# Kernel tuning notes

Measured on AMD Instinct MI355X. Metric: run time of the kernel, lower is better.

## Reference

```python
import jax, jax.numpy as jnp
import numpy as np


def setup_inputs() -> dict:
    key = jax.random.key(0)
    k1, k2, k3 = jax.random.split(key, 3)
    B, C, H, W = 4, 32, 256, 256
    nw, nh = 16, 16
    K = nw * nh
    pixel_feats = jax.random.normal(k1, (B, C, H, W), dtype=jnp.float32)
    assoc_map = jax.random.uniform(k2, (B, 9, H, W), dtype=jnp.float32)
    index_map = jax.random.randint(k3, (B, H, W), 0, K, dtype=jnp.int32)
    return {
        "pixel_feats": pixel_feats,
        "assoc_map": assoc_map,
        "index_map": index_map,
        "nw_spixels": nw,
        "nh_spixels": nh,
    }


def reference(pixel_feats, assoc_map, index_map, nw_spixels, nh_spixels):
    # pixel_feats: [B,C,H,W], assoc_map: [B,9,H,W] (3x3 superpixel-neighbor
    # association weights, row-major (dy,dx) in {-1,0,1}^2), index_map: [B,H,W]
    # base superpixel id in [0, nw*nh). Output: [B, C, nw*nh].
    B, C, H, W = pixel_feats.shape
    K = nw_spixels * nh_spixels
    P = H * W

    idx = index_map.reshape(B, P).astype(jnp.int32)
    ix = idx % nw_spixels  # base spixel grid x
    iy = idx // nw_spixels  # base spixel grid y

    # 9 relative offsets over the superpixel grid
    dy, dx = jnp.meshgrid(jnp.arange(-1, 2), jnp.arange(-1, 2), indexing="ij")
    dy = dy.reshape(9)
    dx = dx.reshape(9)

    tx = ix[:, None, :] + dx[None, :, None]  # [B,9,P]
    ty = iy[:, None, :] + dy[None, :, None]
    valid = (tx >= 0) & (tx < nw_spixels) & (ty >= 0) & (ty < nh_spixels)
    tgt = jnp.where(valid, ty * nw_spixels + tx, 0)  # [B,9,P]

    w = assoc_map.reshape(B, 9, P) * valid.astype(assoc_map.dtype)  # [B,9,P]

    # fold batch into segment id so a single segment_sum handles all images
    seg = (tgt + jnp.arange(B, dtype=jnp.int32)[:, None, None] * K).reshape(-1)

    wsum = jax.ops.segment_sum(w.reshape(-1), seg, num_segments=B * K)  # [B*K]

    # weighted pixel features scattered into superpixel bins
    contrib = w[:, :, None, :] * pixel_feats.reshape(B, 1, C, P)  # [B,9,C,P]
    contrib = contrib.transpose(0, 1, 3, 2).reshape(-1, C)  # [B*9*P, C]
    fsum = jax.ops.segment_sum(contrib, seg, num_segments=B * K)  # [B*K, C]

    eps = 1e-16
    denom = jnp.where(wsum > eps, wsum, 1.0)
    sp = jnp.where(wsum[:, None] > eps, fsum / denom[:, None], 0.0)
    return sp.reshape(B, K, C).transpose(0, 2, 1)  # [B,C,K]
```

## Files before the change

### kernel.cpp

```cpp
#include <hip/hip_runtime.h>
#include <hip/hip_bf16.h>


#define CCH  32
#define TPB  1024
#define PPB  1024
#define STPB 512
#define CAPC 384
#define RECW 24
#define CNTS 16
#define KMAX 256

__device__ __forceinline__ unsigned pack_bf16(float a, float b) {
    unsigned ua = __float_as_uint(a);
    unsigned ub = __float_as_uint(b);
    ua = (ua + 0x7FFFu + ((ua >> 16) & 1u)) >> 16;
    ub = (ub + 0x7FFFu + ((ub >> 16) & 1u)) >> 16;
    return ua | (ub << 16);
}
__device__ __forceinline__ float bf_lo(unsigned u) {
    return __uint_as_float(u << 16);
}
__device__ __forceinline__ float bf_hi(unsigned u) {
    return __uint_as_float(u & 0xFFFF0000u);
}

__global__ __launch_bounds__(TPB, 4) void spx_prep_kernel(
    const float* __restrict__ pf,
    const float* __restrict__ assoc,
    const int*   __restrict__ idxmap,
    const int*   __restrict__ nw_p,
    const int*   __restrict__ nh_p,
    int*         __restrict__ cnt,
    unsigned*    __restrict__ recs,
    float*       __restrict__ fsum,
    int P, int K, int cap, int bpb)
{
    __shared__ int hist[KMAX];
    __shared__ int bases[KMAX];

    const int b   = blockIdx.x / bpb;
    const int blk = blockIdx.x - b * bpb;
    const int tid = threadIdx.x;
    const int p   = blk * PPB + tid;

    if (tid < KMAX) hist[tid] = 0;
    __syncthreads();

    const int*   ix_b = idxmap + (size_t)b * P;
    const float* pf_b = pf     + (size_t)b * CCH * P;
    const float* as_b = assoc  + (size_t)b * 9 * P;

    const int idx  = ix_b[p];
    const int rank = atomicAdd(&hist[idx], 1);

    unsigned u[16];
#pragma unroll
    for (int c2 = 0; c2 < 16; ++c2) {
        const float f0 = pf_b[(size_t)(2*c2  ) * P + p];
        const float f1 = pf_b[(size_t)(2*c2+1) * P + p];
        u[c2] = pack_bf16(f0, f1);
    }
    float wv[9];
#pragma unroll
    for (int j = 0; j < 9; ++j) wv[j] = as_b[(size_t)j * P + p];

    __syncthreads();
    if (tid < KMAX)
        bases[tid] = atomicAdd(&cnt[(b * K + tid) * CNTS], hist[tid]);
    __syncthreads();

    const int pos = bases[idx] + rank;

    if (pos < cap) {
        unsigned* dst = recs + ((size_t)(b * K + idx) * cap + pos) * RECW;
        uint4* d4 = (uint4*)dst;
        d4[0] = make_uint4(u[0],  u[1],  u[2],  u[3]);
        d4[1] = make_uint4(u[4],  u[5],  u[6],  u[7]);
        d4[2] = make_uint4(u[8],  u[9],  u[10], u[11]);
        d4[3] = make_uint4(u[12], u[13], u[14], u[15]);
        d4[4] = make_uint4(pack_bf16(wv[0], wv[1]), pack_bf16(wv[2], wv[3]),
                           pack_bf16(wv[4], wv[5]), pack_bf16(wv[6], wv[7]));
        dst[20] = pack_bf16(wv[8], 0.0f);
    } else {
        const int nw = nw_p[0], nh = nh_p[0];
        const int iy = idx / nw, ixx = idx - (idx / nw) * nw;
#pragma unroll
        for (int j = 0; j < 9; ++j) {
            const int ty = iy + j / 3 - 1, tx = ixx + j % 3 - 1;
            if (tx >= 0 && tx < nw && ty >= 0 && ty < nh) {
                float* o = fsum + (size_t)(b * K + ty * nw + tx) * (CCH + 1);
#pragma unroll
                for (int c2 = 0; c2 < 16; ++c2) {
                    unsafeAtomicAdd(&o[2*c2],     wv[j] * bf_lo(u[c2]));
                    unsafeAtomicAdd(&o[2*c2 + 1], wv[j] * bf_hi(u[c2]));
                }
                unsafeAtomicAdd(&o[CCH], wv[j]);
            }
        }
    }
}

__global__ __launch_bounds__(STPB) void spx_scan_kernel(
    const unsigned* __restrict__ recs,
    const int*      __restrict__ cnt,
    const int*      __restrict__ nw_p,
    const int*      __restrict__ nh_p,
    float*          __restrict__ fsum,
    int K, int cap)
{
    __shared__ float red[32][9][CCH + 1];

    const int bs  = blockIdx.x;
    const int tid = threadIdx.x;
    const int c2  = tid & 15;
    const int g   = tid >> 4;

    int c = cnt[bs * CNTS];
    if (c > cap) c = cap;
    const unsigned* rb = recs + (size_t)bs * cap * RECW;

    float a[9][2], ws9[9];
#pragma unroll
    for (int j = 0; j < 9; ++j) { a[j][0] = 0.f; a[j][1] = 0.f; ws9[j] = 0.f; }

    for (int i = g; i < c; i += 32) {
        const unsigned* r = rb + (size_t)i * RECW;
        const unsigned uf  = r[c2];
        const float f0 = bf_lo(uf), f1 = bf_hi(uf);
        const unsigned wp0 = r[16], wp1 = r[17], wp2 = r[18],
                       wp3 = r[19], wp4 = r[20];
        const float w[9] = { bf_lo(wp0), bf_hi(wp0), bf_lo(wp1), bf_hi(wp1),
                             bf_lo(wp2), bf_hi(wp2), bf_lo(wp3), bf_hi(wp3),
                             bf_lo(wp4) };
#pragma unroll
        for (int j = 0; j < 9; ++j) {
            a[j][0] += w[j] * f0;
            a[j][1] += w[j] * f1;
            ws9[j]  += w[j];
        }
    }

#pragma unroll
    for (int j = 0; j < 9; ++j) {
        red[g][j][2 * c2]     = a[j][0];
        red[g][j][2 * c2 + 1] = a[j][1];
    }
    if (c2 == 0) {
#pragma unroll
        for (int j = 0; j < 9; ++j) red[g][j][CCH] = ws9[j];
    }
    __syncthreads();

    const int b  = bs / K;
    const int s  = bs - b * K;
    const int nw = nw_p[0];
    const int nh = nh_p[0];
    const int sy = s / nw;
    const int sx = s - sy * nw;

    for (int col = tid; col < 9 * (CCH + 1); col += STPB) {
        const int j  = col / (CCH + 1);
        const int cc = col - j * (CCH + 1);
        const int ty = sy + j / 3 - 1;
        const int tx = sx + j % 3 - 1;
        if (tx < 0 || tx >= nw || ty < 0 || ty >= nh) continue;
        float sum = 0.f;
#pragma unroll
        for (int g2 = 0; g2 < 32; ++g2) sum += red[g2][j][cc];
        unsafeAtomicAdd(&fsum[(size_t)(b * K + ty * nw + tx) * (CCH + 1) + cc],
                        sum);
    }
}

__global__ __launch_bounds__(256) void spx_finalize_kernel(
    const float* __restrict__ fsum,
    float*       __restrict__ out,
    int K, int total)
{
    const int gid = blockIdx.x * 256 + threadIdx.x;
    if (gid >= total) return;
    const int k = gid % K;
    const int c = (gid / K) % CCH;
    const int b = gid / (K * CCH);
    const float* f = fsum + (size_t)(b * K + k) * (CCH + 1);
    const float W = f[CCH];
    out[gid] = (W > 1e-16f) ? (f[c] / W) : 0.f;
}

extern "C" void kernel_launch(void* const* d_in, const int* in_sizes, int n_in,
                              void* d_out, int out_size, void* d_ws, size_t ws_size,
                              hipStream_t stream) {
    const float* pf     = (const float*)d_in[0];
    const float* assoc  = (const float*)d_in[1];
    const int*   idxmap = (const int*)d_in[2];
    const int*   nw_p   = (const int*)d_in[3];
    const int*   nh_p   = (const int*)d_in[4];
    float* out = (float*)d_out;

    const int BP = in_sizes[2];
    const int B  = 4;
    const int P  = BP / B;
    const int K  = out_size / (B * CCH);

    const size_t cnt_bytes  = (size_t)B * K * CNTS * sizeof(int);
    const size_t fsum_bytes = (size_t)B * K * (CCH + 1) * sizeof(float);
    int*      cnt  = (int*)d_ws;
    float*    fsum = (float*)((char*)d_ws + cnt_bytes);
    unsigned* recs = (unsigned*)((char*)d_ws + cnt_bytes + fsum_bytes);

    const size_t used  = cnt_bytes + fsum_bytes;
    const size_t avail = (ws_size > used) ? (ws_size - used) : 0;
    int cap = (int)(avail / ((size_t)B * K * RECW * sizeof(unsigned)));
    if (cap > CAPC) cap = CAPC;
    if (cap < 1) cap = 1;

    hipMemsetAsync(cnt, 0, cnt_bytes + fsum_bytes, stream);

    const int bpb = P / PPB;
    spx_prep_kernel<<<B * bpb, TPB, 0, stream>>>(
        pf, assoc, idxmap, nw_p, nh_p, cnt, recs, fsum, P, K, cap, bpb);

    spx_scan_kernel<<<B * K, STPB, 0, stream>>>(
        recs, cnt, nw_p, nh_p, fsum, K, cap);

    const int total = B * K * CCH;
    spx_finalize_kernel<<<(total + 255) / 256, 256, 0, stream>>>(
        fsum, out, K, total);
}
```

Before: 109.9 us.

## Write packed records in pixel order and scatter only pixel indices

```diff
diff --git a/kernel.cpp b/kernel.cpp
--- a/kernel.cpp
+++ b/kernel.cpp
@@ -4,10 +4,9 @@
 
 #define CCH  32
 #define TPB  1024
-#define PPB  1024
 #define STPB 512
 #define CAPC 384
-#define RECW 24
+#define RECW 32
 #define CNTS 16
 #define KMAX 256
 
@@ -33,6 +32,7 @@
     const int*   __restrict__ nh_p,
     int*         __restrict__ cnt,
     unsigned*    __restrict__ recs,
+    int*         __restrict__ pi,
     float*       __restrict__ fsum,
     int P, int K, int cap, int bpb)
 {
@@ -42,7 +42,7 @@
     const int b   = blockIdx.x / bpb;
     const int blk = blockIdx.x - b * bpb;
     const int tid = threadIdx.x;
-    const int p   = blk * PPB + tid;
+    const int p   = blk * TPB + tid;
 
     if (tid < KMAX) hist[tid] = 0;
     __syncthreads();
@@ -65,23 +65,28 @@
 #pragma unroll
     for (int j = 0; j < 9; ++j) wv[j] = as_b[(size_t)j * P + p];
 
-    __syncthreads();
-    if (tid < KMAX)
-        bases[tid] = atomicAdd(&cnt[(b * K + tid) * CNTS], hist[tid]);
-    __syncthreads();
-
-    const int pos = bases[idx] + rank;
-
-    if (pos < cap) {
-        unsigned* dst = recs + ((size_t)(b * K + idx) * cap + pos) * RECW;
-        uint4* d4 = (uint4*)dst;
+    {
+        uint4* d4 = (uint4*)(recs + ((size_t)b * P + p) * RECW);
         d4[0] = make_uint4(u[0],  u[1],  u[2],  u[3]);
         d4[1] = make_uint4(u[4],  u[5],  u[6],  u[7]);
         d4[2] = make_uint4(u[8],  u[9],  u[10], u[11]);
         d4[3] = make_uint4(u[12], u[13], u[14], u[15]);
         d4[4] = make_uint4(pack_bf16(wv[0], wv[1]), pack_bf16(wv[2], wv[3]),
                            pack_bf16(wv[4], wv[5]), pack_bf16(wv[6], wv[7]));
-        dst[20] = pack_bf16(wv[8], 0.0f);
+        d4[5] = make_uint4(pack_bf16(wv[8], 0.0f), 0u, 0u, 0u);
+        d4[6] = make_uint4(0u, 0u, 0u, 0u);
+        d4[7] = make_uint4(0u, 0u, 0u, 0u);
+    }
+
+    __syncthreads();
+    if (tid < KMAX)
+        bases[tid] = atomicAdd(&cnt[(b * K + tid) * CNTS], hist[tid]);
+    __syncthreads();
+
+    const int pos = bases[idx] + rank;
+
+    if (pos < cap) {
+        pi[(size_t)(b * K + idx) * cap + pos] = p;
     } else {
         const int nw = nw_p[0], nh = nh_p[0];
         const int iy = idx / nw, ixx = idx - (idx / nw) * nw;
@@ -103,11 +108,12 @@
 
 __global__ __launch_bounds__(STPB) void spx_scan_kernel(
     const unsigned* __restrict__ recs,
+    const int*      __restrict__ pi,
     const int*      __restrict__ cnt,
     const int*      __restrict__ nw_p,
     const int*      __restrict__ nh_p,
     float*          __restrict__ fsum,
-    int K, int cap)
+    int P, int K, int cap)
 {
     __shared__ float red[32][9][CCH + 1];
 
@@ -118,14 +124,17 @@
 
     int c = cnt[bs * CNTS];
     if (c > cap) c = cap;
-    const unsigned* rb = recs + (size_t)bs * cap * RECW;
+    const int b = bs / K;
+    const int* pib = pi + (size_t)bs * cap;
+    const unsigned* rbase = recs + (size_t)b * P * RECW;
 
     float a[9][2], ws9[9];
 #pragma unroll
     for (int j = 0; j < 9; ++j) { a[j][0] = 0.f; a[j][1] = 0.f; ws9[j] = 0.f; }
 
     for (int i = g; i < c; i += 32) {
-        const unsigned* r = rb + (size_t)i * RECW;
+        const int p = pib[i];
+        const unsigned* r = rbase + (size_t)p * RECW;
         const unsigned uf  = r[c2];
         const float f0 = bf_lo(uf), f1 = bf_hi(uf);
         const unsigned wp0 = r[16], wp1 = r[17], wp2 = r[18],
@@ -152,7 +161,6 @@
     }
     __syncthreads();
 
-    const int b  = bs / K;
     const int s  = bs - b * K;
     const int nw = nw_p[0];
     const int nh = nh_p[0];
@@ -205,24 +213,26 @@
 
     const size_t cnt_bytes  = (size_t)B * K * CNTS * sizeof(int);
     const size_t fsum_bytes = (size_t)B * K * (CCH + 1) * sizeof(float);
+    const size_t recs_bytes = (size_t)BP * RECW * sizeof(unsigned);
     int*      cnt  = (int*)d_ws;
     float*    fsum = (float*)((char*)d_ws + cnt_bytes);
     unsigned* recs = (unsigned*)((char*)d_ws + cnt_bytes + fsum_bytes);
-
-    const size_t used  = cnt_bytes + fsum_bytes;
+    int*      pi   = (int*)((char*)d_ws + cnt_bytes + fsum_bytes + recs_bytes);
+
+    const size_t used  = cnt_bytes + fsum_bytes + recs_bytes;
     const size_t avail = (ws_size > used) ? (ws_size - used) : 0;
-    int cap = (int)(avail / ((size_t)B * K * RECW * sizeof(unsigned)));
+    int cap = (int)(avail / ((size_t)B * K * sizeof(int)));
     if (cap > CAPC) cap = CAPC;
     if (cap < 1) cap = 1;
 
     hipMemsetAsync(cnt, 0, cnt_bytes + fsum_bytes, stream);
 
-    const int bpb = P / PPB;
+    const int bpb = P / TPB;
     spx_prep_kernel<<<B * bpb, TPB, 0, stream>>>(
-        pf, assoc, idxmap, nw_p, nh_p, cnt, recs, fsum, P, K, cap, bpb);
+        pf, assoc, idxmap, nw_p, nh_p, cnt, recs, pi, fsum, P, K, cap, bpb);
 
     spx_scan_kernel<<<B * K, STPB, 0, stream>>>(
-        recs, cnt, nw_p, nh_p, fsum, K, cap);
+        recs, pi, cnt, nw_p, nh_p, fsum, P, K, cap);
 
     const int total = B * K * CCH;
     spx_finalize_kernel<<<(total + 255) / 256, 256, 0, stream>>>(
```

Result: slower. 113.1 us (+2.9%).

## Fuse finalize into scan via completion counters and split record arrays

Applied to the files above, without the earlier changes.

```diff
diff --git a/kernel.cpp b/kernel.cpp
--- a/kernel.cpp
+++ b/kernel.cpp
@@ -4,10 +4,8 @@
 
 #define CCH  32
 #define TPB  1024
-#define PPB  1024
 #define STPB 512
 #define CAPC 384
-#define RECW 24
 #define CNTS 16
 #define KMAX 256
 
@@ -32,7 +30,8 @@
     const int*   __restrict__ nw_p,
     const int*   __restrict__ nh_p,
     int*         __restrict__ cnt,
-    unsigned*    __restrict__ recs,
+    unsigned*    __restrict__ recF,
+    unsigned*    __restrict__ recW,
     float*       __restrict__ fsum,
     int P, int K, int cap, int bpb)
 {
@@ -42,7 +41,7 @@
     const int b   = blockIdx.x / bpb;
     const int blk = blockIdx.x - b * bpb;
     const int tid = threadIdx.x;
-    const int p   = blk * PPB + tid;
+    const int p   = blk * TPB + tid;
 
     if (tid < KMAX) hist[tid] = 0;
     __syncthreads();
@@ -73,15 +72,16 @@
     const int pos = bases[idx] + rank;
 
     if (pos < cap) {
-        unsigned* dst = recs + ((size_t)(b * K + idx) * cap + pos) * RECW;
-        uint4* d4 = (uint4*)dst;
-        d4[0] = make_uint4(u[0],  u[1],  u[2],  u[3]);
-        d4[1] = make_uint4(u[4],  u[5],  u[6],  u[7]);
-        d4[2] = make_uint4(u[8],  u[9],  u[10], u[11]);
-        d4[3] = make_uint4(u[12], u[13], u[14], u[15]);
-        d4[4] = make_uint4(pack_bf16(wv[0], wv[1]), pack_bf16(wv[2], wv[3]),
+        const size_t slot = (size_t)(b * K + idx) * cap + pos;
+        uint4* f4 = (uint4*)(recF + slot * 16);
+        f4[0] = make_uint4(u[0],  u[1],  u[2],  u[3]);
+        f4[1] = make_uint4(u[4],  u[5],  u[6],  u[7]);
+        f4[2] = make_uint4(u[8],  u[9],  u[10], u[11]);
+        f4[3] = make_uint4(u[12], u[13], u[14], u[15]);
+        uint4* w4 = (uint4*)(recW + slot * 8);
+        w4[0] = make_uint4(pack_bf16(wv[0], wv[1]), pack_bf16(wv[2], wv[3]),
                            pack_bf16(wv[4], wv[5]), pack_bf16(wv[6], wv[7]));
-        dst[20] = pack_bf16(wv[8], 0.0f);
+        w4[1] = make_uint4(pack_bf16(wv[8], 0.0f), 0u, 0u, 0u);
     } else {
         const int nw = nw_p[0], nh = nh_p[0];
         const int iy = idx / nw, ixx = idx - (idx / nw) * nw;
@@ -102,14 +102,19 @@
 }
 
 __global__ __launch_bounds__(STPB) void spx_scan_kernel(
-    const unsigned* __restrict__ recs,
+    const unsigned* __restrict__ recF,
+    const unsigned* __restrict__ recW,
     const int*      __restrict__ cnt,
     const int*      __restrict__ nw_p,
     const int*      __restrict__ nh_p,
     float*          __restrict__ fsum,
+    int*            __restrict__ done,
+    float*          __restrict__ out,
     int K, int cap)
 {
     __shared__ float red[32][9][CCH + 1];
+    __shared__ int   win[9];
+    __shared__ float F[CCH + 1];
 
     const int bs  = blockIdx.x;
     const int tid = threadIdx.x;
@@ -118,18 +123,20 @@
 
     int c = cnt[bs * CNTS];
     if (c > cap) c = cap;
-    const unsigned* rb = recs + (size_t)bs * cap * RECW;
+    const int b = bs / K;
+    const unsigned* rF = recF + (size_t)bs * cap * 16;
+    const unsigned* rW = recW + (size_t)bs * cap * 8;
 
     float a[9][2], ws9[9];
 #pragma unroll
     for (int j = 0; j < 9; ++j) { a[j][0] = 0.f; a[j][1] = 0.f; ws9[j] = 0.f; }
 
     for (int i = g; i < c; i += 32) {
-        const unsigned* r = rb + (size_t)i * RECW;
-        const unsigned uf  = r[c2];
+        const unsigned uf = rF[(size_t)i * 16 + c2];
         const float f0 = bf_lo(uf), f1 = bf_hi(uf);
-        const unsigned wp0 = r[16], wp1 = r[17], wp2 = r[18],
-                       wp3 = r[19], wp4 = r[20];
+        const unsigned* rw = rW + (size_t)i * 8;
+        const unsigned wp0 = rw[0], wp1 = rw[1], wp2 = rw[2],
+                       wp3 = rw[3], wp4 = rw[4];
         const float w[9] = { bf_lo(wp0), bf_hi(wp0), bf_lo(wp1), bf_hi(wp1),
                              bf_lo(wp2), bf_hi(wp2), bf_lo(wp3), bf_hi(wp3),
                              bf_lo(wp4) };
@@ -152,7 +159,6 @@
     }
     __syncthreads();
 
-    const int b  = bs / K;
     const int s  = bs - b * K;
     const int nw = nw_p[0];
     const int nh = nh_p[0];
@@ -171,21 +177,44 @@
         unsafeAtomicAdd(&fsum[(size_t)(b * K + ty * nw + tx) * (CCH + 1) + cc],
                         sum);
     }
-}
-
-__global__ __launch_bounds__(256) void spx_finalize_kernel(
-    const float* __restrict__ fsum,
-    float*       __restrict__ out,
-    int K, int total)
-{
-    const int gid = blockIdx.x * 256 + threadIdx.x;
-    if (gid >= total) return;
-    const int k = gid % K;
-    const int c = (gid / K) % CCH;
-    const int b = gid / (K * CCH);
-    const float* f = fsum + (size_t)(b * K + k) * (CCH + 1);
-    const float W = f[CCH];
-    out[gid] = (W > 1e-16f) ? (f[c] / W) : 0.f;
+
+    __syncthreads();
+
+    if (tid < 9) {
+        const int j  = tid;
+        const int ty = sy + j / 3 - 1;
+        const int tx = sx + j % 3 - 1;
+        int w = -1;
+        if (tx >= 0 && tx < nw && ty >= 0 && ty < nh) {
+            const int t    = b * K + ty * nw + tx;
+            const int cnty = 3 - (ty == 0) - (ty == nh - 1);
+            const int cntx = 3 - (tx == 0) - (tx == nw - 1);
+            const int old  = __hip_atomic_fetch_add(
+                &done[t], 1, __ATOMIC_ACQ_REL, __HIP_MEMORY_SCOPE_AGENT);
+            if (old == cnty * cntx - 1) w = t;
+        }
+        win[j] = w;
+    }
+    __syncthreads();
+
+    for (int j = 0; j < 9; ++j) {
+        const int t = win[j];
+        if (t < 0) continue;
+        if (tid < CCH + 1) {
+            F[tid] = __hip_atomic_load(&fsum[(size_t)t * (CCH + 1) + tid],
+                                       __ATOMIC_RELAXED,
+                                       __HIP_MEMORY_SCOPE_AGENT);
+        }
+        __syncthreads();
+        if (tid < CCH) {
+            const float W  = F[CCH];
+            const int   bb = t / K;
+            const int   kk = t - bb * K;
+            out[((size_t)bb * CCH + tid) * K + kk] =
+                (W > 1e-16f) ? (F[tid] / W) : 0.f;
+        }
+        __syncthreads();
+    }
 }
 
 extern "C" void kernel_launch(void* const* d_in, const int* in_sizes, int n_in,
@@ -205,26 +234,26 @@
 
     const size_t cnt_bytes  = (size_t)B * K * CNTS * sizeof(int);
     const size_t fsum_bytes = (size_t)B * K * (CCH + 1) * sizeof(float);
-    int*      cnt  = (int*)d_ws;
-    float*    fsum = (float*)((char*)d_ws + cnt_bytes);
-    unsigned* recs = (unsigned*)((char*)d_ws + cnt_bytes + fsum_bytes);
-
-    const size_t used  = cnt_bytes + fsum_bytes;
-    const size_t avail = (ws_size > used) ? (ws_size - used) : 0;
-    int cap = (int)(avail / ((size_t)B * K * RECW * sizeof(unsigned)));
+    const size_t done_bytes = (size_t)B * K * sizeof(int);
+    int*   cnt  = (int*)d_ws;
+    float* fsum = (float*)((char*)d_ws + cnt_bytes);
+    int*   done = (int*)((char*)d_ws + cnt_bytes + fsum_bytes);
+
+    const size_t head = cnt_bytes + fsum_bytes + done_bytes;
+    const size_t avail = (ws_size > head) ? (ws_size - head) : 0;
+    int cap = (int)(avail / ((size_t)B * K * 24 * sizeof(unsigned)));
     if (cap > CAPC) cap = CAPC;
     if (cap < 1) cap = 1;
 
-    hipMemsetAsync(cnt, 0, cnt_bytes + fsum_bytes, stream);
-
-    const int bpb = P / PPB;
+    unsigned* recF = (unsigned*)((char*)d_ws + head);
+    unsigned* recW = recF + (size_t)B * K * cap * 16;
+
+    hipMemsetAsync(cnt, 0, head, stream);
+
+    const int bpb = P / TPB;
     spx_prep_kernel<<<B * bpb, TPB, 0, stream>>>(
-        pf, assoc, idxmap, nw_p, nh_p, cnt, recs, fsum, P, K, cap, bpb);
+        pf, assoc, idxmap, nw_p, nh_p, cnt, recF, recW, fsum, P, K, cap, bpb);
 
     spx_scan_kernel<<<B * K, STPB, 0, stream>>>(
-        recs, cnt, nw_p, nh_p, fsum, K, cap);
-
-    const int total = B * K * CCH;
-    spx_finalize_kernel<<<(total + 255) / 256, 256, 0, stream>>>(
-        fsum, out, K, total);
-}
+        recF, recW, cnt, nw_p, nh_p, fsum, done, out, K, cap);
+}
```

Measured after the change: 132.1 us. 1.2x slower.
